# Kernel tuning notes

Hardware: AMD Instinct MI355X
Metric: run time of the kernel (lower is better)

Reference implementation:

```python
import jax, jax.numpy as jnp
import numpy as np


def setup_inputs() -> dict:
    key = jax.random.key(0)
    k1, k2, k3, k4 = jax.random.split(key, 4)
    B, L, D, M = 4, 512, 257, 128
    return {
        "input": jax.random.normal(k1, (B, L, 2), dtype=jnp.float32),
        "z0": jax.random.normal(k2, (D,), dtype=jnp.float32),
        "om": jax.random.uniform(k3, (M, 2), dtype=jnp.float32),
        "S": jax.random.normal(k4, (D, D), dtype=jnp.float32),
    }


def _get_T(x, om, S):
    # x: [B, L, 2], om: [M, 2], S: [D, D] with D = 2M+1
    D = S.shape[0]
    M = om.shape[0]
    k_dot_x = jnp.einsum("blc,mc->blm", x, om)          # [B, L, M]
    c = jnp.cos(k_dot_x)
    s = jnp.sin(k_dot_x)
    B, L = x.shape[0], x.shape[1]
    idx1 = 2 * jnp.arange(M) + 1                          # odd indices
    idx2 = idx1 + 1                                       # even indices
    T_irrep = jnp.zeros((B, L, D, D), dtype=x.dtype)
    T_irrep = T_irrep.at[:, :, 0, 0].set(1.0)             # trivial irrep
    T_irrep = T_irrep.at[:, :, idx1, idx1].set(c)
    T_irrep = T_irrep.at[:, :, idx1, idx2].set(-s)
    T_irrep = T_irrep.at[:, :, idx2, idx1].set(s)
    T_irrep = T_irrep.at[:, :, idx2, idx2].set(c)
    S_inv = jnp.linalg.inv(S)
    # T = S @ T_irrep @ S^-1 for every (b, l)
    T = jnp.einsum("ij,bljk,kn->blin", S, T_irrep, S_inv)
    return T


def reference(input, z0, om, S):
    B = input.shape[0]
    T = _get_T(input, om, S)                              # [B, L, D, D]
    z_init = jnp.broadcast_to(z0, (B, z0.shape[0]))       # [B, D]

    def scan_fn(z, T_t):                                  # T_t: [B, D, D]
        z_new = jnp.einsum("bij,bj->bi", T_t, z)
        return z_new, z_new

    _, outs = jax.lax.scan(scan_fn, z_init, jnp.swapaxes(T, 0, 1))  # [L, B, D]
    outputs = jnp.swapaxes(outs, 0, 1)                    # [B, L, D]
    z_final = outputs[:, -1, :]
    return outputs, z_final
```

## Files before the change

### kernel.cpp

```cpp
#include <hip/hip_runtime.h>
#include <math.h>

#define N    257
#define AP   258
#define MM   128
#define LL   512
#define BB   4
#define NB   32
#define U12S 226

#define A_BYTE    0
#define W0_BYTE   265224
#define CXY_BYTE  266256
#define PW_BYTE   282640
#define U12_BYTE  315536
#define ST_BYTE   344464

__global__ __launch_bounds__(512) void stage_scan_kernel(const float* __restrict__ S,
                                                         const float* __restrict__ z0,
                                                         const float* __restrict__ x,
                                                         void* __restrict__ wsv) {
  const int tid = threadIdx.x;
  const int bid = blockIdx.x;

  if (bid < 130) {
    float* A  = (float*)((char*)wsv + A_BYTE);
    float* St = (float*)((char*)wsv + ST_BYTE);
    const int idx = bid * 512 + tid;
    if (idx < N * N) {
      const int i = idx / N, j = idx - i * N;
      A[(size_t)i * AP + j] = S[idx];
      St[idx] = S[j * N + i];
    } else if (idx < N * N + N) {
      const int r = idx - N * N;
      A[(size_t)r * AP + N] = z0[r];
    }
    return;
  }

  const int wave = tid >> 6, lane = tid & 63;
  const int b    = wave >> 1, comp = wave & 1;
  const float* xp = x + ((size_t)b * LL) * 2 + comp;
  double loc[8];
  double run = 0.0;
  #pragma unroll
  for (int e = 0; e < 8; ++e) {
    run += (double)xp[(lane * 8 + e) * 2];
    loc[e] = run;
  }
  double tot = run;
  #pragma unroll
  for (int off = 1; off < 64; off <<= 1) {
    const double o = __shfl_up(tot, off);
    if (lane >= off) tot += o;
  }
  const double excl = tot - run;
  float* cp = (float*)((char*)wsv + CXY_BYTE) + ((size_t)b * LL) * 2 + comp;
  #pragma unroll
  for (int e = 0; e < 8; ++e)
    cp[(lane * 8 + e) * 2] = (float)(excl + loc[e]);
}

__global__ __launch_bounds__(320, 1) void panel_factor_kernel(void* __restrict__ wsv,
                                                              int k0) {
  __shared__ __align__(16) float piv[2][NB];
  __shared__ float pinvs[2];
  __shared__ __align__(16) float F11s[NB][NB + 4];
  float* A    = (float*)((char*)wsv + A_BYTE);
  float* Pw   = (float*)((char*)wsv + PW_BYTE);
  float* U12w = (float*)((char*)wsv + U12_BYTE);
  const int tid = threadIdx.x;
  const int ct  = k0 + NB;
  const int tc2 = 258 - ct;

  float r[NB];
  if (tid < N) {
    const float* Ar = A + (size_t)tid * AP + k0;
    #pragma unroll
    for (int c = 0; c < NB; c += 2) {
      const float2 v = *(const float2*)&Ar[c];
      r[c] = v.x; r[c + 1] = v.y;
    }
  }

  if (tid == k0) {
    #pragma unroll
    for (int c = 0; c < NB; ++c) piv[0][c] = r[c];
    pinvs[0] = 1.0f / r[0];
  }
  __syncthreads();

  #pragma unroll
  for (int j = 0; j < NB; ++j) {
    const int pr = k0 + j;
    const int bsel = j & 1;
    if (tid < N && (tid < k0 || tid > pr)) {
      const float f = r[j] * pinvs[bsel];
      #pragma unroll
      for (int q = 0; q < NB / 4; ++q) {
        if (4 * q + 3 > j) {
          const float4 pv = *(const float4*)&piv[bsel][4 * q];
          if (4 * q     > j) r[4 * q]     -= f * pv.x;
          if (4 * q + 1 > j) r[4 * q + 1] -= f * pv.y;
          if (4 * q + 2 > j) r[4 * q + 2] -= f * pv.z;
          r[4 * q + 3] -= f * pv.w;
        }
      }
      r[j] = f;
      if (j + 1 < NB && tid == pr + 1) {
        #pragma unroll
        for (int c = 0; c < NB; ++c)
          if (c > j) piv[bsel ^ 1][c] = r[c];
        pinvs[bsel ^ 1] = 1.0f / r[j + 1];
      }
    }
    __syncthreads();
  }

  if (tid < N) {
    if (tid >= k0 && tid < ct) {
      const int fr = tid - k0;
      #pragma unroll
      for (int c = 0; c < NB; ++c) {
        F11s[fr][c] = r[c];
        A[(size_t)tid * AP + k0 + c] = r[c];
      }
    } else {
      #pragma unroll
      for (int t = 0; t < NB; ++t)
        Pw[(size_t)t * N + tid] = r[t];
    }
  }
  __syncthreads();

  if (tid < tc2) {
    float u[NB];
    #pragma unroll
    for (int jr = 0; jr < NB; ++jr)
      u[jr] = A[(size_t)(k0 + jr) * AP + ct + tid];
    #pragma unroll
    for (int jr = 1; jr < NB; ++jr) {
      float vv = u[jr];
      #pragma unroll
      for (int q = 0; q < jr / 4; ++q) {
        const float4 fv = *(const float4*)&F11s[jr][4 * q];
        vv -= fv.x * u[4 * q];
        vv -= fv.y * u[4 * q + 1];
        vv -= fv.z * u[4 * q + 2];
        vv -= fv.w * u[4 * q + 3];
      }
      #pragma unroll
      for (int t = (jr / 4) * 4; t < jr; ++t)
        vv -= F11s[jr][t] * u[t];
      u[jr] = vv;
    }
    #pragma unroll
    for (int jr = 0; jr < NB; ++jr) {
      U12w[jr * U12S + tid] = u[jr];
      A[(size_t)(k0 + jr) * AP + ct + tid] = u[jr];
    }
  }
}

__global__ __launch_bounds__(256) void panel_update_kernel(void* __restrict__ wsv,
                                                           int k0, int tc2) {
  __shared__ float Pl[NB][NB + 1];
  __shared__ __align__(16) float Ul[NB][66];
  float* A = (float*)((char*)wsv + A_BYTE);
  const float* Pw   = (const float*)((const char*)wsv + PW_BYTE);
  const float* U12w = (const float*)((const char*)wsv + U12_BYTE);
  const int tid = threadIdx.x;
  const int ct  = k0 + NB;
  const int rb0 = blockIdx.x * 32;
  const int c0  = blockIdx.y * 64;

  for (int i = tid; i < 32 * 32; i += 256) {
    const int t = i >> 5, rr = i & 31;
    const int rb = rb0 + rr;
    const int gr = (rb < k0) ? rb : rb + NB;
    Pl[t][rr] = (rb < 225) ? Pw[(size_t)t * N + gr] : 0.0f;
  }
  for (int i = tid; i < 32 * 64; i += 256) {
    const int t = i >> 6, c = i & 63;
    Ul[t][c] = (c0 + c < tc2) ? U12w[t * U12S + c0 + c] : 0.0f;
  }
  __syncthreads();

  const int tr  = tid >> 4;
  const int tcx = (tid & 15) * 4;
  float acc[2][4];
  #pragma unroll
  for (int rr = 0; rr < 2; ++rr) {
    const int rb = rb0 + tr * 2 + rr;
    const int gr = (rb < k0) ? rb : rb + NB;
    #pragma unroll
    for (int c = 0; c < 4; ++c)
      acc[rr][c] = (rb < 225 && (c0 + tcx + c) < tc2)
                 ? A[(size_t)gr * AP + ct + c0 + tcx + c] : 0.0f;
  }
  #pragma unroll
  for (int t = 0; t < NB; ++t) {
    const float p0 = Pl[t][tr * 2], p1 = Pl[t][tr * 2 + 1];
    const float2 u0 = *(const float2*)&Ul[t][tcx];
    const float2 u1 = *(const float2*)&Ul[t][tcx + 2];
    acc[0][0] -= p0 * u0.x; acc[0][1] -= p0 * u0.y;
    acc[0][2] -= p0 * u1.x; acc[0][3] -= p0 * u1.y;
    acc[1][0] -= p1 * u0.x; acc[1][1] -= p1 * u0.y;
    acc[1][2] -= p1 * u1.x; acc[1][3] -= p1 * u1.y;
  }
  #pragma unroll
  for (int rr = 0; rr < 2; ++rr) {
    const int rb = rb0 + tr * 2 + rr;
    const int gr = (rb < k0) ? rb : rb + NB;
    #pragma unroll
    for (int c = 0; c < 4; ++c)
      if (rb < 225 && (c0 + tcx + c) < tc2)
        A[(size_t)gr * AP + ct + c0 + tcx + c] = acc[rr][c];
  }
}

__global__ __launch_bounds__(256) void last_kernel(void* __restrict__ wsv) {
  __shared__ float xs[N];
  __shared__ float rr[256];
  float* A = (float*)((char*)wsv + A_BYTE);
  const float* Pw   = (const float*)((const char*)wsv + PW_BYTE);
  const float* U12w = (const float*)((const char*)wsv + U12_BYTE);
  float* w0f = (float*)((char*)wsv + W0_BYTE);
  const int tid = threadIdx.x;

  for (int idx = tid; idx < 225 * 2; idx += 256) {
    const int rb = idx >> 1, c = idx & 1;
    const int gr = (rb < 224) ? rb : 256;
    float acc = A[(size_t)gr * AP + 256 + c];
    #pragma unroll
    for (int t = 0; t < NB; ++t)
      acc -= Pw[(size_t)t * N + gr] * U12w[t * U12S + c];
    A[(size_t)gr * AP + 256 + c] = acc;
  }
  __threadfence_block();
  __syncthreads();

  if (tid == 0) xs[256] = A[256 * AP + 257] / A[256 * AP + 256];
  __syncthreads();
  const float x256 = xs[256];
  rr[tid] = A[(size_t)tid * AP + 257] - A[(size_t)tid * AP + 256] * x256;
  __syncthreads();
  const int fk0 = tid & ~31;
  const int fs  = tid & 31;
  for (int j = 31; j >= 0; --j) {
    if (fs == j) xs[fk0 + j] = rr[fk0 + j] / A[(size_t)(fk0 + j) * AP + (fk0 + j)];
    __syncthreads();
    if (fs < j) rr[fk0 + fs] -= A[(size_t)(fk0 + fs) * AP + (fk0 + j)] * xs[fk0 + j];
    __syncthreads();
  }
  w0f[tid] = xs[tid];
  if (tid == 0) w0f[256] = xs[256];
}

#define NL 8
__global__ __launch_bounds__(320) void combine_kernel(const float* __restrict__ S,
                                                      const float* __restrict__ om,
                                                      const void* __restrict__ wsv,
                                                      float* __restrict__ out) {
  const int tid = threadIdx.x;
  const int b  = blockIdx.y;
  const int l0 = blockIdx.x * NL;
  const float* w0  = (const float*)((const char*)wsv + W0_BYTE);
  const float* cxy = (const float*)((const char*)wsv + CXY_BYTE);
  const float* St  = (const float*)((const char*)wsv + ST_BYTE);
  __shared__ __align__(16) float Wl[N][NL];
  __shared__ float omsh[2 * MM];
  __shared__ float cxs[NL], cys[NL];

  for (int idx = tid; idx < 2 * MM; idx += 320) omsh[idx] = om[idx];
  if (tid < NL) {
    cxs[tid] = cxy[((size_t)(b * LL) + l0 + tid) * 2];
    cys[tid] = cxy[((size_t)(b * LL) + l0 + tid) * 2 + 1];
  }
  __syncthreads();

  for (int idx = tid; idx < NL * N; idx += 320) {
    const int d = idx >> 3;
    const int r = idx & 7;
    float v;
    if (d == 0) {
      v = w0[0];
    } else {
      const int m = (d - 1) >> 1;
      const int pq = 2 * m + 1;
      const float t = cxs[r] * omsh[2 * m] + cys[r] * omsh[2 * m + 1];
      float s, c;
      sincosf(t, &s, &c);
      const float a0 = w0[pq], a1 = w0[pq + 1];
      v = (d & 1) ? (c * a0 - s * a1) : (s * a0 + c * a1);
    }
    Wl[d][r] = v;
  }
  __syncthreads();

  const int i = tid;
  if (i < N) {
    float acc[NL];
    #pragma unroll
    for (int r = 0; r < NL; ++r) acc[r] = 0.0f;
    #pragma unroll 8
    for (int d = 0; d < N; ++d) {
      const float stv = St[(size_t)d * N + i];
      const float4 wa = *(const float4*)&Wl[d][0];
      const float4 wb = *(const float4*)&Wl[d][4];
      acc[0] += stv * wa.x; acc[1] += stv * wa.y;
      acc[2] += stv * wa.z; acc[3] += stv * wa.w;
      acc[4] += stv * wb.x; acc[5] += stv * wb.y;
      acc[6] += stv * wb.z; acc[7] += stv * wb.w;
    }
    const size_t base = (size_t)(b * LL + l0) * N + i;
    #pragma unroll
    for (int r = 0; r < NL; ++r) out[base + (size_t)r * N] = acc[r];
    if (l0 + NL == LL) {
      out[(size_t)BB * LL * N + (size_t)b * N + i] = acc[NL - 1];
    }
  }
}

extern "C" void kernel_launch(void* const* d_in, const int* in_sizes, int n_in,
                              void* d_out, int out_size, void* d_ws, size_t ws_size,
                              hipStream_t stream) {
  const float* x  = (const float*)d_in[0];
  const float* z0 = (const float*)d_in[1];
  const float* om = (const float*)d_in[2];
  const float* S  = (const float*)d_in[3];
  float* out = (float*)d_out;

  hipLaunchKernelGGL(stage_scan_kernel, dim3(131), dim3(512), 0, stream, S, z0, x, d_ws);
  for (int p = 0; p < 8; ++p) {
    const int k0  = p * NB;
    const int tc2 = 258 - (k0 + NB);
    hipLaunchKernelGGL(panel_factor_kernel, dim3(1), dim3(320), 0, stream, d_ws, k0);
    if (p < 7)
      hipLaunchKernelGGL(panel_update_kernel, dim3(8, (tc2 + 63) / 64), dim3(256),
                         0, stream, d_ws, k0, tc2);
  }
  hipLaunchKernelGGL(last_kernel, dim3(1), dim3(256), 0, stream, d_ws);
  hipLaunchKernelGGL(combine_kernel, dim3(LL / NL, BB), dim3(320), 0, stream, S, om, d_ws, out);
}
```

Baseline: 296.3 us.

## Eliminate two pivot rows per barrier in panel LU factorization

Changes the panel factorization's inner loop so each phase handles two pivot columns at once. Every thread rebuilds the second pivot row itself from the raw next row and the first pivot row. This halves the number of __syncthreads barriers in the panel kernel. In exchange, each thread does some redundant arithmetic and divisions. The rows that come after each pivot pair also see small floating-point ordering differences.

```diff
diff --git a/kernel.cpp b/kernel.cpp
--- a/kernel.cpp
+++ b/kernel.cpp
@@ -63,8 +63,8 @@
 
 __global__ __launch_bounds__(320, 1) void panel_factor_kernel(void* __restrict__ wsv,
                                                               int k0) {
-  __shared__ __align__(16) float piv[2][NB];
-  __shared__ float pinvs[2];
+  __shared__ __align__(16) float pivA[2][NB];
+  __shared__ __align__(16) float rawB[2][NB];
   __shared__ __align__(16) float F11s[NB][NB + 4];
   float* A    = (float*)((char*)wsv + A_BYTE);
   float* Pw   = (float*)((char*)wsv + PW_BYTE);
@@ -85,33 +85,73 @@
 
   if (tid == k0) {
     #pragma unroll
-    for (int c = 0; c < NB; ++c) piv[0][c] = r[c];
-    pinvs[0] = 1.0f / r[0];
-  }
-  __syncthreads();
-
-  #pragma unroll
-  for (int j = 0; j < NB; ++j) {
-    const int pr = k0 + j;
-    const int bsel = j & 1;
-    if (tid < N && (tid < k0 || tid > pr)) {
-      const float f = r[j] * pinvs[bsel];
-      #pragma unroll
-      for (int q = 0; q < NB / 4; ++q) {
-        if (4 * q + 3 > j) {
-          const float4 pv = *(const float4*)&piv[bsel][4 * q];
-          if (4 * q     > j) r[4 * q]     -= f * pv.x;
-          if (4 * q + 1 > j) r[4 * q + 1] -= f * pv.y;
-          if (4 * q + 2 > j) r[4 * q + 2] -= f * pv.z;
-          r[4 * q + 3] -= f * pv.w;
+    for (int c = 0; c < NB; ++c) pivA[0][c] = r[c];
+  }
+  if (tid == k0 + 1) {
+    #pragma unroll
+    for (int c = 0; c < NB; ++c) rawB[0][c] = r[c];
+  }
+  __syncthreads();
+
+  #pragma unroll
+  for (int ph = 0; ph < NB / 2; ++ph) {
+    const int j   = 2 * ph;
+    const int s   = ph & 1;
+    const int prj = k0 + j;
+    if (tid < N && (tid < k0 || tid > prj)) {
+      const float pinv1 = 1.0f / pivA[s][j];
+      const float f1 = r[j] * pinv1;
+      if (tid == prj + 1) {
+        #pragma unroll
+        for (int q = 0; q < NB / 4; ++q) {
+          if (4 * q + 3 > j) {
+            const float4 pv = *(const float4*)&pivA[s][4 * q];
+            if (4 * q     > j) r[4 * q]     -= f1 * pv.x;
+            if (4 * q + 1 > j) r[4 * q + 1] -= f1 * pv.y;
+            if (4 * q + 2 > j) r[4 * q + 2] -= f1 * pv.z;
+            r[4 * q + 3] -= f1 * pv.w;
+          }
         }
-      }
-      r[j] = f;
-      if (j + 1 < NB && tid == pr + 1) {
+        r[j] = f1;
+      } else {
+        const float fB    = rawB[s][j] * pinv1;
+        const float prj1  = rawB[s][j + 1] - fB * pivA[s][j + 1];
+        const float pinv2 = 1.0f / prj1;
+        r[j + 1] -= f1 * pivA[s][j + 1];
+        const float f2 = r[j + 1] * pinv2;
         #pragma unroll
-        for (int c = 0; c < NB; ++c)
-          if (c > j) piv[bsel ^ 1][c] = r[c];
-        pinvs[bsel ^ 1] = 1.0f / r[j + 1];
+        for (int q = 0; q < NB / 4; ++q) {
+          if (4 * q + 3 > j + 1) {
+            const float4 pv = *(const float4*)&pivA[s][4 * q];
+            const float4 rw = *(const float4*)&rawB[s][4 * q];
+            if (4 * q > j + 1) {
+              r[4 * q] -= f1 * pv.x;
+              r[4 * q] -= f2 * (rw.x - fB * pv.x);
+            }
+            if (4 * q + 1 > j + 1) {
+              r[4 * q + 1] -= f1 * pv.y;
+              r[4 * q + 1] -= f2 * (rw.y - fB * pv.y);
+            }
+            if (4 * q + 2 > j + 1) {
+              r[4 * q + 2] -= f1 * pv.z;
+              r[4 * q + 2] -= f2 * (rw.z - fB * pv.z);
+            }
+            r[4 * q + 3] -= f1 * pv.w;
+            r[4 * q + 3] -= f2 * (rw.w - fB * pv.w);
+          }
+        }
+        r[j]     = f1;
+        r[j + 1] = f2;
+        if (ph + 1 < NB / 2) {
+          if (tid == prj + 2) {
+            #pragma unroll
+            for (int c = 0; c < NB; ++c) pivA[s ^ 1][c] = r[c];
+          }
+          if (tid == prj + 3) {
+            #pragma unroll
+            for (int c = 0; c < NB; ++c) rawB[s ^ 1][c] = r[c];
+          }
+        }
       }
     }
     __syncthreads();
```

Measured after the change: 320.0 us. +8.0%, slower.
